# Kernel tuning notes

Hardware: AMD Instinct MI355X
Metric: run time of the kernel (lower is better)

Reference implementation:

```python
import jax, jax.numpy as jnp
import numpy as np

N = 100000          # nodes
E = 1_600_000       # edges (nnz of sparse adj)
IN_F = 256
OUT_F = 128
DROP_P = 0.2


def setup_inputs() -> dict:
    key = jax.random.key(0)
    k1, k2, k3, k4, k5, k6 = jax.random.split(key, 6)
    return {
        "input": jax.random.normal(k1, (N, IN_F), dtype=jnp.float32),
        "weight": jax.random.normal(k2, (IN_F, OUT_F), dtype=jnp.float32) * 0.05,
        "adj_row": jax.random.randint(k3, (E,), 0, N, dtype=jnp.int32),
        "adj_col": jax.random.randint(k4, (E,), 0, N, dtype=jnp.int32),
        "adj_val": jax.random.uniform(k5, (E,), dtype=jnp.float32),
        "drop_u": jax.random.uniform(k6, (N, IN_F), dtype=jnp.float32),
    }


def reference(input, weight, adj_row, adj_col, adj_val, drop_u):
    # F.dropout(input, p, training=True): zero with prob p, scale survivors by 1/(1-p)
    x = jnp.where(drop_u > DROP_P, input / (1.0 - DROP_P), 0.0)
    # dense projection: [N, in] @ [in, out] -> [N, out]
    support = x @ weight
    # SpMM: out[r] = sum over edges e with row==r of val[e] * support[col[e]]
    gathered = support[adj_col] * adj_val[:, None]          # [E, out]
    output = jax.ops.segment_sum(gathered, adj_row, num_segments=N)  # [N, out]
    return output
```

## Files before the change

kernel.cpp:

```cpp
#include <hip/hip_runtime.h>

#define N_NODES 100000
#define IN_F 256
#define OUT_F 128
#define NB 782
#define CAP 2560
#define QCAP 896
#define TILE 4096
#define BPAD 42

typedef __attribute__((ext_vector_type(8))) short v8s;
typedef __attribute__((ext_vector_type(4))) float v4f;

__device__ __forceinline__ unsigned short f2bf(float f) {
    unsigned int u = __float_as_uint(f);
    u += 0x7fffu + ((u >> 16) & 1u);
    return (unsigned short)(u >> 16);
}
__device__ __forceinline__ float bf2f(unsigned short s) {
    return __uint_as_float((unsigned int)s << 16);
}

__global__ void wt_kernel(const float* __restrict__ w, unsigned short* __restrict__ bt) {
    int idx = blockIdx.x * 256 + threadIdx.x;
    int k = idx >> 7;
    int n = idx & 127;
    bt[n * IN_F + k] = f2bf(w[idx]);
}

__global__ __launch_bounds__(256) void gemm_kernel(
    const float* __restrict__ x, const float* __restrict__ u,
    const unsigned short* __restrict__ bt, unsigned short* __restrict__ support) {
    __shared__ unsigned short Bs[2][128 * BPAD];

    const int tid  = threadIdx.x;
    const int lane = tid & 63;
    const int wv   = tid >> 6;
    const int cl   = lane & 15;
    const int kq   = lane >> 4;
    const long long row = (long long)blockIdx.x * 64 + wv * 16 + cl;
    const bool rv = row < N_NODES;
    const long long rowc = rv ? row : (N_NODES - 1);
    const float* xs = x + rowc * IN_F + kq * 8;
    const float* us = u + rowc * IN_F + kq * 8;
    const float m = rv ? 1.25f : 0.0f;

    const int scol = tid >> 1;
    const int skh  = (tid & 1) * 16;
    const unsigned short* bsrc = bt + scol * IN_F + skh;
    unsigned short* bdst0 = &Bs[0][scol * BPAD + skh];
    unsigned short* bdst1 = &Bs[1][scol * BPAD + skh];

    v4f acc[8] = {};

    *(v8s*)(bdst0)     = *(const v8s*)(bsrc);
    *(v8s*)(bdst0 + 8) = *(const v8s*)(bsrc + 8);
    __syncthreads();

    #pragma unroll
    for (int s = 0; s < 8; ++s) {
        const int k0 = s * 32;
        float4 x0 = *(const float4*)(xs + k0);
        float4 x1 = *(const float4*)(xs + k0 + 4);
        float4 u0 = *(const float4*)(us + k0);
        float4 u1 = *(const float4*)(us + k0 + 4);
        if (s < 7) {
            const unsigned short* src = bsrc + (s + 1) * 32;
            unsigned short* dst = (s & 1) ? bdst0 : bdst1;
            *(v8s*)(dst)     = *(const v8s*)(src);
            *(v8s*)(dst + 8) = *(const v8s*)(src + 8);
        }
        const unsigned short* bb = (s & 1) ? &Bs[1][0] : &Bs[0][0];
        v8s bf[8];
        #pragma unroll
        for (int tn = 0; tn < 8; ++tn)
            bf[tn] = *(const v8s*)&bb[(tn * 16 + cl) * BPAD + kq * 8];
        unsigned short t0 = f2bf(u0.x > 0.2f ? x0.x * m : 0.0f);
        unsigned short t1 = f2bf(u0.y > 0.2f ? x0.y * m : 0.0f);
        unsigned short t2 = f2bf(u0.z > 0.2f ? x0.z * m : 0.0f);
        unsigned short t3 = f2bf(u0.w > 0.2f ? x0.w * m : 0.0f);
        unsigned short t4 = f2bf(u1.x > 0.2f ? x1.x * m : 0.0f);
        unsigned short t5 = f2bf(u1.y > 0.2f ? x1.y * m : 0.0f);
        unsigned short t6 = f2bf(u1.z > 0.2f ? x1.z * m : 0.0f);
        unsigned short t7 = f2bf(u1.w > 0.2f ? x1.w * m : 0.0f);
        v8s af = {(short)t0, (short)t1, (short)t2, (short)t3,
                  (short)t4, (short)t5, (short)t6, (short)t7};
        #pragma unroll
        for (int tn = 0; tn < 8; ++tn)
            acc[tn] = __builtin_amdgcn_mfma_f32_16x16x32_bf16(af, bf[tn], acc[tn], 0, 0, 0);
        __syncthreads();
    }

    const int rq = lane >> 4;
    #pragma unroll
    for (int r = 0; r < 4; ++r) {
        long long g = (long long)blockIdx.x * 64 + wv * 16 + rq * 4 + r;
        if (g < N_NODES) {
            unsigned short* o = support + g * OUT_F + cl;
            #pragma unroll
            for (int tn = 0; tn < 8; ++tn)
                o[tn * 16] = f2bf(acc[tn][r]);
        }
    }
}

__global__ void init_kernel(int* __restrict__ cursor) {
    int i = blockIdx.x * 256 + threadIdx.x;
    if (i < NB) cursor[i * 16] = i * CAP;
}

__global__ __launch_bounds__(256) void scatter_kernel(
    const int* __restrict__ row, const int* __restrict__ col,
    const float* __restrict__ val, int* __restrict__ cursor,
    int2* __restrict__ cv, int E) {
    __shared__ int cnt[1024];
    __shared__ int loc[1024];
    __shared__ int delta[1024];
    __shared__ int tmp[256];
    __shared__ int gd[TILE];
    __shared__ int2 stage[TILE];
    __shared__ int total_s;
    const int tid = threadIdx.x;
    const int base_e = blockIdx.x * TILE;

    for (int i = tid; i < 1024; i += 256) cnt[i] = 0;
    __syncthreads();
    #pragma unroll
    for (int j = 0; j < TILE / 256; ++j) {
        int e = base_e + j * 256 + tid;
        if (e < E) atomicAdd(&cnt[row[e] >> 7], 1);
    }
    __syncthreads();
    int c0 = cnt[4*tid], c1 = cnt[4*tid+1], c2 = cnt[4*tid+2], c3 = cnt[4*tid+3];
    int s = c0 + c1 + c2 + c3;
    tmp[tid] = s;
    __syncthreads();
    #pragma unroll
    for (int d = 1; d < 256; d <<= 1) {
        int t = (tid >= d) ? tmp[tid - d] : 0;
        __syncthreads();
        tmp[tid] += t;
        __syncthreads();
    }
    int excl = tmp[tid] - s;
    loc[4*tid]   = excl;
    loc[4*tid+1] = excl + c0;
    loc[4*tid+2] = excl + c0 + c1;
    loc[4*tid+3] = excl + c0 + c1 + c2;
    if (tid == 255) total_s = tmp[255];
    __syncthreads();
    for (int i = tid; i < NB; i += 256) {
        int c = cnt[i];
        int gbase = 0;
        if (c > 0) gbase = atomicAdd(&cursor[i * 16], c);
        delta[i] = gbase - loc[i];
        cnt[i] = loc[i];
    }
    __syncthreads();
    #pragma unroll
    for (int j = 0; j < TILE / 256; ++j) {
        int e = base_e + j * 256 + tid;
        if (e < E) {
            int r = row[e];
            int b = r >> 7;
            int rank = atomicAdd(&cnt[b], 1);
            stage[rank] = make_int2(col[e] | ((r & 127) << 17), __float_as_int(val[e]));
            gd[rank] = delta[b] + rank;
        }
    }
    __syncthreads();
    int total = total_s;
    for (int i = tid; i < total; i += 256)
        cv[gd[i]] = stage[i];
}

__global__ __launch_bounds__(256) void acc2_kernel(
    const int* __restrict__ cursor, const int2* __restrict__ cv,
    const unsigned short* __restrict__ support, float* __restrict__ out) {
    __shared__ int2 sorted[QCAP];
    __shared__ int cnt_s[32];
    __shared__ int start_s[32];
    __shared__ int pos_s[32];
    const int tid = threadIdx.x;
    const int bq = blockIdx.x;
    const int b = bq >> 2;
    const int q = bq & 3;
    const int e0 = b * CAP;
    const int nE = cursor[b * 16] - e0;

    if (tid < 32) cnt_s[tid] = 0;
    __syncthreads();
    int2 ej[10];
    int  vj[10];
    #pragma unroll
    for (int j = 0; j < 10; ++j) {
        int i = j * 256 + tid;
        int2 c = cv[e0 + i];
        int lr = (c.x >> 17) & 127;
        int mine = (i < nE) && ((lr >> 5) == q);
        ej[j] = c;
        vj[j] = mine ? (lr & 31) : -1;
        if (mine) atomicAdd(&cnt_s[lr & 31], 1);
    }
    __syncthreads();
    if (tid < 32) {
        int v = cnt_s[tid];
        int sc = v;
        #pragma unroll
        for (int d = 1; d < 32; d <<= 1) {
            int t = __shfl_up(sc, d, 64);
            if (tid >= d) sc += t;
        }
        start_s[tid] = sc - v;
        pos_s[tid] = sc - v;
    }
    __syncthreads();
    #pragma unroll
    for (int j = 0; j < 10; ++j) {
        if (vj[j] >= 0) {
            int rank = atomicAdd(&pos_s[vj[j]], 1);
            sorted[rank] = ej[j];
        }
    }
    __syncthreads();
    const int lane = tid & 63, w = tid >> 6;
    const long long rowbase = (long long)b * 128 + q * 32;
    for (int rr = 0; rr < 8; ++rr) {
        int rl = w * 8 + rr;
        int e = start_s[rl];
        int end = e + cnt_s[rl];
        float a0 = 0.f, a1 = 0.f;
        for (; e < end; e += 4) {
            #pragma unroll
            for (int j = 0; j < 4; ++j) {
                int idx = e + j;
                int ids = min(idx, end - 1);
                int2 c = sorted[ids];
                float vv = (idx < end) ? __int_as_float(c.y) : 0.0f;
                int colv = c.x & 131071;
                unsigned int uu = *(const unsigned int*)(support + colv * OUT_F + lane * 2);
                a0 = fmaf(vv, bf2f((unsigned short)(uu & 0xffff)), a0);
                a1 = fmaf(vv, bf2f((unsigned short)(uu >> 16)), a1);
            }
        }
        long long g = rowbase + rl;
        if (g < N_NODES)
            *(float2*)(out + g * OUT_F + lane * 2) = make_float2(a0, a1);
    }
}

extern "C" void kernel_launch(void* const* d_in, const int* in_sizes, int n_in,
                              void* d_out, int out_size, void* d_ws, size_t ws_size,
                              hipStream_t stream) {
    const float* input   = (const float*)d_in[0];
    const float* weight  = (const float*)d_in[1];
    const int*   adj_row = (const int*)d_in[2];
    const int*   adj_col = (const int*)d_in[3];
    const float* adj_val = (const float*)d_in[4];
    const float* drop_u  = (const float*)d_in[5];
    float* out = (float*)d_out;
    const int E = in_sizes[2];

    char* p = (char*)d_ws;
    unsigned short* bt      = (unsigned short*)p;  p += 65536;
    int2*           cv      = (int2*)p;            p += (size_t)NB * CAP * sizeof(int2);
    unsigned short* support = (unsigned short*)p;  p += (size_t)N_NODES * OUT_F * 2;
    int*            cursor  = (int*)p;

    init_kernel<<<4, 256, 0, stream>>>(cursor);
    wt_kernel<<<128, 256, 0, stream>>>(weight, bt);
    gemm_kernel<<<(N_NODES + 63) / 64, 256, 0, stream>>>(input, drop_u, bt, support);
    scatter_kernel<<<(E + TILE - 1) / TILE, 256, 0, stream>>>(adj_row, adj_col, adj_val, cursor, cv, E);
    acc2_kernel<<<NB * 4, 256, 0, stream>>>(cursor, cv, support, out);
}
```

Baseline: 384.2 us.

## Load GEMM weights directly from global with two-stage register prefetch; unroll SpMM gather by eight

The GEMM kernel drops the shared-memory double buffer for the transposed weight along with its per-step barriers. Each wave now loads its B fragments straight from global memory (L2/L1 cached) into registers, with a two-stage software prefetch of the x, u and B operands. The SpMM inner loop is unrolled to eight edges per iteration so more gathers are in flight. This raises register pressure and repeats weight fetches per wave. The wider SpMM unroll also wastes clamped loads on rows with few edges.

```diff
diff --git a/kernel.cpp b/kernel.cpp
--- a/kernel.cpp
+++ b/kernel.cpp
@@ -7,7 +7,6 @@
 #define CAP 2560
 #define QCAP 896
 #define TILE 4096
-#define BPAD 42
 
 typedef __attribute__((ext_vector_type(8))) short v8s;
 typedef __attribute__((ext_vector_type(4))) float v4f;
@@ -31,8 +30,6 @@
 __global__ __launch_bounds__(256) void gemm_kernel(
     const float* __restrict__ x, const float* __restrict__ u,
     const unsigned short* __restrict__ bt, unsigned short* __restrict__ support) {
-    __shared__ unsigned short Bs[2][128 * BPAD];
-
     const int tid  = threadIdx.x;
     const int lane = tid & 63;
     const int wv   = tid >> 6;
@@ -44,52 +41,60 @@
     const float* xs = x + rowc * IN_F + kq * 8;
     const float* us = u + rowc * IN_F + kq * 8;
     const float m = rv ? 1.25f : 0.0f;
-
-    const int scol = tid >> 1;
-    const int skh  = (tid & 1) * 16;
-    const unsigned short* bsrc = bt + scol * IN_F + skh;
-    unsigned short* bdst0 = &Bs[0][scol * BPAD + skh];
-    unsigned short* bdst1 = &Bs[1][scol * BPAD + skh];
+    const unsigned short* bb = bt + cl * IN_F + kq * 8;
 
     v4f acc[8] = {};
-
-    *(v8s*)(bdst0)     = *(const v8s*)(bsrc);
-    *(v8s*)(bdst0 + 8) = *(const v8s*)(bsrc + 8);
-    __syncthreads();
-
-    #pragma unroll
-    for (int s = 0; s < 8; ++s) {
-        const int k0 = s * 32;
-        float4 x0 = *(const float4*)(xs + k0);
-        float4 x1 = *(const float4*)(xs + k0 + 4);
-        float4 u0 = *(const float4*)(us + k0);
-        float4 u1 = *(const float4*)(us + k0 + 4);
-        if (s < 7) {
-            const unsigned short* src = bsrc + (s + 1) * 32;
-            unsigned short* dst = (s & 1) ? bdst0 : bdst1;
-            *(v8s*)(dst)     = *(const v8s*)(src);
-            *(v8s*)(dst + 8) = *(const v8s*)(src + 8);
-        }
-        const unsigned short* bb = (s & 1) ? &Bs[1][0] : &Bs[0][0];
-        v8s bf[8];
-        #pragma unroll
-        for (int tn = 0; tn < 8; ++tn)
-            bf[tn] = *(const v8s*)&bb[(tn * 16 + cl) * BPAD + kq * 8];
-        unsigned short t0 = f2bf(u0.x > 0.2f ? x0.x * m : 0.0f);
-        unsigned short t1 = f2bf(u0.y > 0.2f ? x0.y * m : 0.0f);
-        unsigned short t2 = f2bf(u0.z > 0.2f ? x0.z * m : 0.0f);
-        unsigned short t3 = f2bf(u0.w > 0.2f ? x0.w * m : 0.0f);
-        unsigned short t4 = f2bf(u1.x > 0.2f ? x1.x * m : 0.0f);
-        unsigned short t5 = f2bf(u1.y > 0.2f ? x1.y * m : 0.0f);
-        unsigned short t6 = f2bf(u1.z > 0.2f ? x1.z * m : 0.0f);
-        unsigned short t7 = f2bf(u1.w > 0.2f ? x1.w * m : 0.0f);
-        v8s af = {(short)t0, (short)t1, (short)t2, (short)t3,
-                  (short)t4, (short)t5, (short)t6, (short)t7};
-        #pragma unroll
-        for (int tn = 0; tn < 8; ++tn)
-            acc[tn] = __builtin_amdgcn_mfma_f32_16x16x32_bf16(af, bf[tn], acc[tn], 0, 0, 0);
-        __syncthreads();
-    }
+    float4 xa0A, xa1A, ua0A, ua1A, xa0B, xa1B, ua0B, ua1B;
+    v8s bfA[8], bfB[8];
+
+#define LA(s, X0, X1, U0, U1) \
+    X0 = *(const float4*)(xs + (s) * 32); \
+    X1 = *(const float4*)(xs + (s) * 32 + 4); \
+    U0 = *(const float4*)(us + (s) * 32); \
+    U1 = *(const float4*)(us + (s) * 32 + 4)
+
+#define LB(s, BF) \
+    _Pragma("unroll") \
+    for (int tn = 0; tn < 8; ++tn) \
+        BF[tn] = *(const v8s*)(bb + tn * 16 * IN_F + (s) * 32)
+
+#define STEP(s, X0, X1, U0, U1, BF) \
+    { \
+        float4 x0 = X0, x1 = X1, u0 = U0, u1 = U1; \
+        v8s bf[8]; \
+        _Pragma("unroll") \
+        for (int tn = 0; tn < 8; ++tn) bf[tn] = BF[tn]; \
+        if ((s) < 6) { LA((s) + 2, X0, X1, U0, U1); LB((s) + 2, BF); } \
+        unsigned short t0 = f2bf(u0.x > 0.2f ? x0.x * m : 0.0f); \
+        unsigned short t1 = f2bf(u0.y > 0.2f ? x0.y * m : 0.0f); \
+        unsigned short t2 = f2bf(u0.z > 0.2f ? x0.z * m : 0.0f); \
+        unsigned short t3 = f2bf(u0.w > 0.2f ? x0.w * m : 0.0f); \
+        unsigned short t4 = f2bf(u1.x > 0.2f ? x1.x * m : 0.0f); \
+        unsigned short t5 = f2bf(u1.y > 0.2f ? x1.y * m : 0.0f); \
+        unsigned short t6 = f2bf(u1.z > 0.2f ? x1.z * m : 0.0f); \
+        unsigned short t7 = f2bf(u1.w > 0.2f ? x1.w * m : 0.0f); \
+        v8s af = {(short)t0, (short)t1, (short)t2, (short)t3, \
+                  (short)t4, (short)t5, (short)t6, (short)t7}; \
+        _Pragma("unroll") \
+        for (int tn = 0; tn < 8; ++tn) \
+            acc[tn] = __builtin_amdgcn_mfma_f32_16x16x32_bf16(af, bf[tn], acc[tn], 0, 0, 0); \
+    }
+
+    LA(0, xa0A, xa1A, ua0A, ua1A); LB(0, bfA);
+    LA(1, xa0B, xa1B, ua0B, ua1B); LB(1, bfB);
+
+    STEP(0, xa0A, xa1A, ua0A, ua1A, bfA);
+    STEP(1, xa0B, xa1B, ua0B, ua1B, bfB);
+    STEP(2, xa0A, xa1A, ua0A, ua1A, bfA);
+    STEP(3, xa0B, xa1B, ua0B, ua1B, bfB);
+    STEP(4, xa0A, xa1A, ua0A, ua1A, bfA);
+    STEP(5, xa0B, xa1B, ua0B, ua1B, bfB);
+    STEP(6, xa0A, xa1A, ua0A, ua1A, bfA);
+    STEP(7, xa0B, xa1B, ua0B, ua1B, bfB);
+
+#undef LA
+#undef LB
+#undef STEP
 
     const int rq = lane >> 4;
     #pragma unroll
@@ -230,9 +235,9 @@
         int e = start_s[rl];
         int end = e + cnt_s[rl];
         float a0 = 0.f, a1 = 0.f;
-        for (; e < end; e += 4) {
+        for (; e < end; e += 8) {
             #pragma unroll
-            for (int j = 0; j < 4; ++j) {
+            for (int j = 0; j < 8; ++j) {
                 int idx = e + j;
                 int ids = min(idx, end - 1);
                 int2 c = sorted[ids];
```

After: 401.5 us. 1.05x slower.
